# Kernel tuning notes

Hardware: AMD Instinct MI355X
Metric: run time of the kernel (lower is better)

## Reference

```python
import jax, jax.numpy as jnp
import numpy as np

N_NODES = 100000
N_EDGES = 1600000
DIM = 128
N_LAYERS = 4


def setup_inputs() -> dict:
    key = jax.random.key(0)
    ks = jax.random.split(key, 6)
    h = jax.random.normal(ks[0], (N_NODES, DIM), dtype=jnp.float32)
    src = jax.random.randint(ks[1], (N_EDGES,), 0, N_NODES, dtype=jnp.int32)
    dst = jax.random.randint(ks[2], (N_EDGES,), 0, N_NODES, dtype=jnp.int32)
    scale = 1.0 / np.sqrt(DIM)
    W_embed = jax.random.normal(ks[3], (DIM, DIM), dtype=jnp.float32) * scale
    b_embed = jnp.zeros((DIM,), dtype=jnp.float32)
    Ws = jax.random.normal(ks[4], (N_LAYERS, DIM, DIM), dtype=jnp.float32) * scale
    bs = jnp.zeros((N_LAYERS, DIM), dtype=jnp.float32)
    return {"h": h, "src": src, "dst": dst, "W_embed": W_embed,
            "b_embed": b_embed, "Ws": Ws, "bs": bs}


def reference(h, src, dst, W_embed, b_embed, Ws, bs):
    # Symmetric GCN normalization (DGL GraphConv norm='both'):
    # out-degree on src side, in-degree on dst side, clamped to >= 1.
    ones = jnp.ones(src.shape, h.dtype)
    deg_out = jax.ops.segment_sum(ones, src, num_segments=N_NODES)
    deg_in = jax.ops.segment_sum(ones, dst, num_segments=N_NODES)
    norm_s = jax.lax.rsqrt(jnp.maximum(deg_out, 1.0))  # [N]
    norm_d = jax.lax.rsqrt(jnp.maximum(deg_in, 1.0))   # [N]

    # embedding_h (dropout p=0 -> identity)
    h = h @ W_embed + b_embed

    for i in range(N_LAYERS):
        h_in = h
        # gather -> scale -> scatter-add (A_norm @ h)
        m = h[src] * norm_s[src, None]                              # [E, D]
        agg = jax.ops.segment_sum(m, dst, num_segments=N_NODES)    # [N, D]
        z = (agg * norm_d[:, None]) @ Ws[i] + bs[i]                 # GraphConv weight+bias
        z = jax.nn.relu(z)                                          # activation
        h = h_in + z                                                # residual
    return h
```

## Files before the change

kernel.cpp:

```cpp
#include <hip/hip_runtime.h>

#define DIMN 128
#define NLAYERS 4
#define KP 136
#define WTSH (2 * DIMN * KP)

#define BQL 9
#define BUCKW 512
#define BUCKCAP 10240
#define BSCH 4096
#define NBUK_MAX 256

#define HP_P 3
#define HP_C 48
#define HIST_BLOCKS (HP_P * HP_C)
#define HW_WORDS 16667

typedef __attribute__((ext_vector_type(8))) short bf16x8;
typedef __attribute__((ext_vector_type(4))) float f32x4;

__device__ inline float bfu2f(unsigned int u) { return __uint_as_float(u << 16); }
__device__ inline unsigned short f2bf(float f) {
    unsigned int u = __float_as_uint(f);
    return (unsigned short)((u + 0x7fffu + ((u >> 16) & 1u)) >> 16);
}
__device__ inline float blo(unsigned int u) { return __uint_as_float(u << 16); }
__device__ inline float bhi(unsigned int u) { return __uint_as_float(u & 0xffff0000u); }

__global__ __launch_bounds__(256) void k_pre(const int* __restrict__ src,
                                             const float* __restrict__ We,
                                             const float* __restrict__ Wlayers,
                                             unsigned int* __restrict__ degOutP,
                                             short* __restrict__ wt, int N, int E) {
    __shared__ unsigned int hsm[HW_WORDS];
    int tid = threadIdx.x;
    int bid = blockIdx.x;

    if (bid < HIST_BLOCKS) {
        int c = bid / HP_P;
        int p = bid % HP_P;
        int W = (N + 1) / 2;
        int w0 = p * HW_WORDS;
        int wn = min(HW_WORDS, W - w0);
        if (wn <= 0) return;
        int per = ((E + HP_C - 1) / HP_C + 3) & ~3;
        int e0 = c * per;
        int e1 = min(e0 + per, E);
        if (e0 >= e1) {
            for (int i = tid; i < wn; i += 256) degOutP[(size_t)c * W + w0 + i] = 0u;
            return;
        }
        for (int i = tid; i < wn; i += 256) hsm[i] = 0u;
        __syncthreads();
        int nvec = (e1 - e0) >> 2;
        const int4* sv = (const int4*)(src + e0);
        for (int it = tid; it < nvec; it += 256) {
            int4 v = sv[it];
            int w;
            w = (v.x >> 1) - w0; if ((unsigned)w < (unsigned)wn) atomicAdd(&hsm[w], 1u << ((v.x & 1) << 4));
            w = (v.y >> 1) - w0; if ((unsigned)w < (unsigned)wn) atomicAdd(&hsm[w], 1u << ((v.y & 1) << 4));
            w = (v.z >> 1) - w0; if ((unsigned)w < (unsigned)wn) atomicAdd(&hsm[w], 1u << ((v.z & 1) << 4));
            w = (v.w >> 1) - w0; if ((unsigned)w < (unsigned)wn) atomicAdd(&hsm[w], 1u << ((v.w & 1) << 4));
        }
        for (int j = e0 + (nvec << 2) + tid; j < e1; j += 256) {
            int s = src[j];
            int w = (s >> 1) - w0;
            if ((unsigned)w < (unsigned)wn) atomicAdd(&hsm[w], 1u << ((s & 1) << 4));
        }
        __syncthreads();
        for (int i = tid; i < wn; i += 256) degOutP[(size_t)c * W + w0 + i] = hsm[i];
        return;
    }

    {
        int m = bid - HIST_BLOCKS;
        const float* Wm = (m == 0) ? We : Wlayers + (size_t)(m - 1) * DIMN * DIMN;
        short* o = wt + (size_t)m * WTSH;
#pragma unroll
        for (int it = 0; it < 16; ++it) {
            int f = it * 1024 + tid * 4;
            float4 v = *(const float4*)(Wm + f);
            int k = f >> 7, n = f & 127;
            float vv[4] = {v.x, v.y, v.z, v.w};
#pragma unroll
            for (int j = 0; j < 4; ++j) {
                unsigned short hb = f2bf(vv[j]);
                float lo = vv[j] - bfu2f(hb);
                o[(n + j) * KP + k] = (short)hb;
                o[DIMN * KP + (n + j) * KP + k] = (short)f2bf(lo);
            }
        }
    }
}

__global__ __launch_bounds__(256) void k_binsort(const int* __restrict__ src,
                                                 const int* __restrict__ dst,
                                                 int* __restrict__ gcur,
                                                 int2* __restrict__ pairs,
                                                 int E, int NBUK) {
    __shared__ int cnt[NBUK_MAX];
    __shared__ int bofs[NBUK_MAX];
    __shared__ int gof[NBUK_MAX];
    __shared__ int scan_s[256];
    __shared__ int2 stg[BSCH];
    int tid = threadIdx.x;
    int e0 = blockIdx.x * BSCH;
    int n = min(BSCH, E - e0);
    if (n <= 0) return;
    cnt[tid] = 0;
    __syncthreads();

    int nv = n >> 2;
    const int4* dv4 = (const int4*)(dst + e0);
    for (int it = tid; it < nv; it += 256) {
        int4 d = dv4[it];
        atomicAdd(&cnt[d.x >> BQL], 1);
        atomicAdd(&cnt[d.y >> BQL], 1);
        atomicAdd(&cnt[d.z >> BQL], 1);
        atomicAdd(&cnt[d.w >> BQL], 1);
    }
    for (int j = (nv << 2) + tid; j < n; j += 256) {
        atomicAdd(&cnt[dst[e0 + j] >> BQL], 1);
    }
    __syncthreads();

    int myc = cnt[tid];
    scan_s[tid] = myc;
    __syncthreads();
    for (int off = 1; off < 256; off <<= 1) {
        int x = scan_s[tid];
        if (tid >= off) x += scan_s[tid - off];
        __syncthreads();
        scan_s[tid] = x;
        __syncthreads();
    }
    bofs[tid] = scan_s[tid] - myc;
    gof[tid] = (myc > 0 && tid < NBUK) ? atomicAdd(&gcur[tid], myc) : 0;
    cnt[tid] = 0;
    __syncthreads();

    const int4* sv4 = (const int4*)(src + e0);
    for (int it = tid; it < nv; it += 256) {
        int4 d = dv4[it];
        int4 s = sv4[it];
        int b, p;
        b = d.x >> BQL; p = bofs[b] + atomicAdd(&cnt[b], 1); stg[p] = make_int2(s.x, d.x);
        b = d.y >> BQL; p = bofs[b] + atomicAdd(&cnt[b], 1); stg[p] = make_int2(s.y, d.y);
        b = d.z >> BQL; p = bofs[b] + atomicAdd(&cnt[b], 1); stg[p] = make_int2(s.z, d.z);
        b = d.w >> BQL; p = bofs[b] + atomicAdd(&cnt[b], 1); stg[p] = make_int2(s.w, d.w);
    }
    for (int j = (nv << 2) + tid; j < n; j += 256) {
        int d = dst[e0 + j], s = src[e0 + j];
        int b = d >> BQL;
        int p = bofs[b] + atomicAdd(&cnt[b], 1);
        stg[p] = make_int2(s, d);
    }
    __syncthreads();

    for (int i = tid; i < n; i += 256) {
        int2 pr = stg[i];
        int b = pr.y >> BQL;
        int go = gof[b] + (i - bofs[b]);
        if (go < BUCKCAP) pairs[(size_t)b * BUCKCAP + go] = pr;
    }
}

__global__ __launch_bounds__(256) void k_build(const int2* __restrict__ pairs,
                                               const int* __restrict__ gcur,
                                               int* __restrict__ csr,
                                               int* __restrict__ rowptr,
                                               int* __restrict__ deg, int N) {
    int b = blockIdx.x;
    int tid = threadIdx.x;
    int cntb = gcur[b];
    if (cntb > BUCKCAP) cntb = BUCKCAP;
    __shared__ int c[BUCKW];
    __shared__ int pf[BUCKW];
    c[tid] = 0; c[tid + 256] = 0;
    __syncthreads();
    const int2* bp = pairs + (size_t)b * BUCKCAP;
    for (int i = tid; i < cntb; i += 256) atomicAdd(&c[bp[i].y & (BUCKW - 1)], 1);
    __syncthreads();
    pf[tid] = c[tid]; pf[tid + 256] = c[tid + 256];
    __syncthreads();
    for (int off = 1; off < BUCKW; off <<= 1) {
        int i0 = tid, i1 = tid + 256;
        int v0 = pf[i0] + ((i0 >= off) ? pf[i0 - off] : 0);
        int v1 = pf[i1] + ((i1 >= off) ? pf[i1 - off] : 0);
        __syncthreads();
        pf[i0] = v0; pf[i1] = v1;
        __syncthreads();
    }
    {
        int i0 = tid, i1 = tid + 256;
        int c0 = c[i0], c1 = c[i1];
        int ex0 = pf[i0] - c0, ex1 = pf[i1] - c1;
        pf[i0] = ex0; pf[i1] = ex1;
        int gn0 = (b << BQL) + i0, gn1 = (b << BQL) + i1;
        if (gn0 < N) { rowptr[gn0] = b * BUCKCAP + ex0; deg[gn0] = c0; }
        if (gn1 < N) { rowptr[gn1] = b * BUCKCAP + ex1; deg[gn1] = c1; }
        c[i0] = 0; c[i1] = 0;
    }
    __syncthreads();
    int* cb = csr + (size_t)b * BUCKCAP;
    for (int i = tid; i < cntb; i += 256) {
        int2 p = bp[i];
        int ld = p.y & (BUCKW - 1);
        int pos = pf[ld] + atomicAdd(&c[ld], 1);
        cb[pos] = p.x;
    }
}

__global__ __launch_bounds__(256) void k_norms(const int* __restrict__ deg,
                                               const unsigned int* __restrict__ degOutP,
                                               float* __restrict__ norm_d,
                                               float* __restrict__ norm_s, int N) {
    int i = blockIdx.x * 256 + threadIdx.x;
    int W = (N + 1) / 2;
    if (i < W) {
        unsigned s0 = 0, s1 = 0;
#pragma unroll 8
        for (int c = 0; c < HP_C; ++c) {
            unsigned v = degOutP[(size_t)c * W + i];
            s0 += v & 0xffffu;
            s1 += v >> 16;
        }
        int n0 = 2 * i, n1 = 2 * i + 1;
        norm_s[n0] = rsqrtf(fmaxf((float)s0, 1.0f));
        norm_d[n0] = rsqrtf(fmaxf((float)deg[n0], 1.0f));
        if (n1 < N) {
            norm_s[n1] = rsqrtf(fmaxf((float)s1, 1.0f));
            norm_d[n1] = rsqrtf(fmaxf((float)deg[n1], 1.0f));
        }
    }
}

__global__ __launch_bounds__(512) void k_gemm_f32(const float* __restrict__ A,
                                                  const short* __restrict__ Wt,
                                                  const float* __restrict__ bg,
                                                  float* __restrict__ tgt,
                                                  const float* __restrict__ norm_s,
                                                  unsigned short* __restrict__ Hs, int N) {
    __shared__ short Wl[WTSH];
    __shared__ float bias_s[DIMN];
    int tid = threadIdx.x;
    {
        const uint4* g = (const uint4*)Wt;
        uint4* l = (uint4*)Wl;
#pragma unroll
        for (int it = 0; it < 9; ++it) {
            int ix = it * 512 + tid;
            if (ix < WTSH / 8) l[ix] = g[ix];
        }
        if (tid < DIMN) bias_s[tid] = bg[tid];
    }
    __syncthreads();

    int lane = tid & 63;
    int wv = tid >> 6;
    int quad = lane >> 4;
    int l15 = lane & 15;
    int row0 = blockIdx.x * 256 + wv * 32;

    f32x4 acc[2][8];
#pragma unroll
    for (int s = 0; s < 2; ++s)
#pragma unroll
        for (int ct = 0; ct < 8; ++ct) acc[s][ct] = (f32x4){0.f, 0.f, 0.f, 0.f};

    for (int ks = 0; ks < 4; ++ks) {
        int kb = ks * 32 + quad * 8;
        bf16x8 ah[2], al[2];
#pragma unroll
        for (int s = 0; s < 2; ++s) {
            int r = row0 + s * 16 + l15;
            if (r > N - 1) r = N - 1;
            const float* ap = A + (size_t)r * DIMN + kb;
            float4 p = *(const float4*)ap;
            float4 q = *(const float4*)(ap + 4);
            float fv[8] = {p.x, p.y, p.z, p.w, q.x, q.y, q.z, q.w};
#pragma unroll
            for (int j = 0; j < 8; ++j) {
                unsigned short hb = f2bf(fv[j]);
                ah[s][j] = (short)hb;
                al[s][j] = (short)f2bf(fv[j] - bfu2f(hb));
            }
        }
#pragma unroll
        for (int ct = 0; ct < 8; ++ct) {
            const short* bp = Wl + (ct * 16 + l15) * KP + kb;
            bf16x8 bh = *(const bf16x8*)bp;
            bf16x8 bl = *(const bf16x8*)(bp + DIMN * KP);
#pragma unroll
            for (int s = 0; s < 2; ++s) {
                acc[s][ct] = __builtin_amdgcn_mfma_f32_16x16x32_bf16(ah[s], bh, acc[s][ct], 0, 0, 0);
                acc[s][ct] = __builtin_amdgcn_mfma_f32_16x16x32_bf16(al[s], bh, acc[s][ct], 0, 0, 0);
                acc[s][ct] = __builtin_amdgcn_mfma_f32_16x16x32_bf16(ah[s], bl, acc[s][ct], 0, 0, 0);
            }
        }
    }

#pragma unroll
    for (int s = 0; s < 2; ++s) {
        int rbase = row0 + s * 16 + quad * 4;
        float ns[4];
#pragma unroll
        for (int rj = 0; rj < 4; ++rj) {
            int row = rbase + rj;
            ns[rj] = (row < N) ? norm_s[row] : 0.f;
        }
#pragma unroll
        for (int ct = 0; ct < 8; ++ct) {
            int col = ct * 16 + l15;
            float bv = bias_s[col];
#pragma unroll
            for (int rj = 0; rj < 4; ++rj) {
                int row = rbase + rj;
                if (row < N) {
                    float o = acc[s][ct][rj] + bv;
                    __builtin_nontemporal_store(o, &tgt[(size_t)row * DIMN + col]);
                    Hs[(size_t)row * DIMN + col] = f2bf(o * ns[rj]);
                }
            }
        }
    }
}

__global__ __launch_bounds__(512) void k_gemm_bf(const unsigned short* __restrict__ A,
                                                 const short* __restrict__ Wt,
                                                 const float* __restrict__ bg,
                                                 const float* __restrict__ Hres,
                                                 float* __restrict__ tgt,
                                                 const float* __restrict__ norm_s,
                                                 unsigned short* __restrict__ Hs, int N) {
    __shared__ short Wl[WTSH];
    __shared__ float bias_s[DIMN];
    int tid = threadIdx.x;
    {
        const uint4* g = (const uint4*)Wt;
        uint4* l = (uint4*)Wl;
#pragma unroll
        for (int it = 0; it < 9; ++it) {
            int ix = it * 512 + tid;
            if (ix < WTSH / 8) l[ix] = g[ix];
        }
        if (tid < DIMN) bias_s[tid] = bg[tid];
    }
    __syncthreads();

    int lane = tid & 63;
    int wv = tid >> 6;
    int quad = lane >> 4;
    int l15 = lane & 15;
    int row0 = blockIdx.x * 256 + wv * 32;

    f32x4 acc[2][8];
#pragma unroll
    for (int s = 0; s < 2; ++s)
#pragma unroll
        for (int ct = 0; ct < 8; ++ct) acc[s][ct] = (f32x4){0.f, 0.f, 0.f, 0.f};

    for (int ks = 0; ks < 4; ++ks) {
        int kb = ks * 32 + quad * 8;
        bf16x8 ah[2];
#pragma unroll
        for (int s = 0; s < 2; ++s) {
            int r = row0 + s * 16 + l15;
            if (r > N - 1) r = N - 1;
            ah[s] = *(const bf16x8*)(A + (size_t)r * DIMN + kb);
        }
#pragma unroll
        for (int ct = 0; ct < 8; ++ct) {
            const short* bp = Wl + (ct * 16 + l15) * KP + kb;
            bf16x8 bh = *(const bf16x8*)bp;
            bf16x8 bl = *(const bf16x8*)(bp + DIMN * KP);
#pragma unroll
            for (int s = 0; s < 2; ++s) {
                acc[s][ct] = __builtin_amdgcn_mfma_f32_16x16x32_bf16(ah[s], bh, acc[s][ct], 0, 0, 0);
                acc[s][ct] = __builtin_amdgcn_mfma_f32_16x16x32_bf16(ah[s], bl, acc[s][ct], 0, 0, 0);
            }
        }
    }

    bool doHs = (Hs != nullptr);
#pragma unroll
    for (int s = 0; s < 2; ++s) {
        int rbase = row0 + s * 16 + quad * 4;
        float ns[4];
        if (doHs) {
#pragma unroll
            for (int rj = 0; rj < 4; ++rj) {
                int row = rbase + rj;
                ns[rj] = (row < N) ? norm_s[row] : 0.f;
            }
        }
#pragma unroll
        for (int ct = 0; ct < 8; ++ct) {
            int col = ct * 16 + l15;
            float bv = bias_s[col];
#pragma unroll
            for (int rj = 0; rj < 4; ++rj) {
                int row = rbase + rj;
                if (row < N) {
                    float o = fmaxf(acc[s][ct][rj] + bv, 0.f) + Hres[(size_t)row * DIMN + col];
                    __builtin_nontemporal_store(o, &tgt[(size_t)row * DIMN + col]);
                    if (doHs) Hs[(size_t)row * DIMN + col] = f2bf(o * ns[rj]);
                }
            }
        }
    }
}

__global__ __launch_bounds__(256) void k_spmm(const unsigned int* __restrict__ Hs,
                                              unsigned short* __restrict__ AggB,
                                              const int* __restrict__ csr,
                                              const int* __restrict__ rowptr,
                                              const int* __restrict__ deg,
                                              const float* __restrict__ norm_d, int N) {
    int wave = (blockIdx.x * blockDim.x + threadIdx.x) >> 6;
    int lane = threadIdx.x & 63;
    if (wave >= N) return;
    int cnt = deg[wave];
    const int* base = csr + rowptr[wave];
    int g = lane >> 5;
    int l5 = lane & 31;
    const uint2* H2 = (const uint2*)Hs;
    float4 acc = make_float4(0.f, 0.f, 0.f, 0.f);

    int emain = cnt & ~7;
    int e = 0;
    for (; e < emain; e += 8) {
        int s0 = base[e + g];
        int s1 = base[e + 2 + g];
        int s2 = base[e + 4 + g];
        int s3 = base[e + 6 + g];
        uint2 h0 = H2[(size_t)s0 * 32 + l5];
        uint2 h1 = H2[(size_t)s1 * 32 + l5];
        uint2 h2 = H2[(size_t)s2 * 32 + l5];
        uint2 h3 = H2[(size_t)s3 * 32 + l5];
        acc.x += blo(h0.x); acc.y += bhi(h0.x);
        acc.z += blo(h0.y); acc.w += bhi(h0.y);
        acc.x += blo(h1.x); acc.y += bhi(h1.x);
        acc.z += blo(h1.y); acc.w += bhi(h1.y);
        acc.x += blo(h2.x); acc.y += bhi(h2.x);
        acc.z += blo(h2.y); acc.w += bhi(h2.y);
        acc.x += blo(h3.x); acc.y += bhi(h3.x);
        acc.z += blo(h3.y); acc.w += bhi(h3.y);
    }
    for (; e < cnt; e += 2) {
        int ee = e + g;
        int sc = base[min(ee, cnt - 1)];
        uint2 hv = H2[(size_t)sc * 32 + l5];
        if (ee < cnt) {
            acc.x += blo(hv.x); acc.y += bhi(hv.x);
            acc.z += blo(hv.y); acc.w += bhi(hv.y);
        }
    }
    acc.x += __shfl_xor(acc.x, 32);
    acc.y += __shfl_xor(acc.y, 32);
    acc.z += __shfl_xor(acc.z, 32);
    acc.w += __shfl_xor(acc.w, 32);
    if (g == 0) {
        float nd = norm_d[wave];
        unsigned long long p =
            (unsigned long long)((unsigned)f2bf(acc.x * nd) | ((unsigned)f2bf(acc.y * nd) << 16)) |
            ((unsigned long long)((unsigned)f2bf(acc.z * nd) | ((unsigned)f2bf(acc.w * nd) << 16)) << 32);
        __builtin_nontemporal_store(p, &((unsigned long long*)AggB)[(size_t)wave * 32 + l5]);
    }
}

static inline char* align256(char* p) {
    return (char*)(((uintptr_t)p + 255) & ~(uintptr_t)255);
}

extern "C" void kernel_launch(void* const* d_in, const int* in_sizes, int n_in,
                              void* d_out, int out_size, void* d_ws, size_t ws_size,
                              hipStream_t stream) {
    const float* h_in = (const float*)d_in[0];
    const int* src = (const int*)d_in[1];
    const int* dst = (const int*)d_in[2];
    const float* W_embed = (const float*)d_in[3];
    const float* b_embed = (const float*)d_in[4];
    const float* Ws = (const float*)d_in[5];
    const float* bs = (const float*)d_in[6];
    float* out = (float*)d_out;

    const int N = in_sizes[0] / DIMN;
    const int E = in_sizes[1];
    const int W = (N + 1) / 2;
    const int NBUK = (N + BUCKW - 1) >> BQL;

    char* w = (char*)d_ws;
    float* Hc = (float*)w;               w = align256(w + (size_t)N * DIMN * 4);
    unsigned short* AggB = (unsigned short*)w; w = align256(w + (size_t)N * DIMN * 2);
    unsigned short* Hs = (unsigned short*)w;   w = align256(w + (size_t)N * DIMN * 2);
    int2* pairs = (int2*)w;              w = align256(w + (size_t)NBUK * BUCKCAP * 8);
    int* csr = (int*)w;                  w = align256(w + (size_t)NBUK * BUCKCAP * 4);
    int* rowptr = (int*)w;               w = align256(w + (size_t)N * 4);
    int* deg = (int*)w;                  w = align256(w + (size_t)N * 4);
    int* gcur = (int*)w;                 w = align256(w + (size_t)NBUK * 4);
    unsigned int* degOutP = (unsigned int*)w;  w = align256(w + (size_t)HP_C * W * 4);
    float* norm_s = (float*)w;           w = align256(w + (size_t)N * 4);
    float* norm_d = (float*)w;           w = align256(w + (size_t)N * 4);
    short* wt = (short*)w;               w = align256(w + (size_t)5 * WTSH * 2);

    (void)hipMemsetAsync(gcur, 0, (size_t)NBUK * 4, stream);

    int gb = (N + 255) / 256;
    int nb = (W + 255) / 256;
    int bb = (E + BSCH - 1) / BSCH;

    k_pre<<<HIST_BLOCKS + 5, 256, 0, stream>>>(src, W_embed, Ws, degOutP, wt, N, E);

    k_binsort<<<bb, 256, 0, stream>>>(src, dst, gcur, pairs, E, NBUK);
    k_build<<<NBUK, 256, 0, stream>>>(pairs, gcur, csr, rowptr, deg, N);

    k_norms<<<nb, 256, 0, stream>>>(deg, degOutP, norm_d, norm_s, N);

    k_gemm_f32<<<gb, 512, 0, stream>>>(h_in, wt, b_embed, Hc, norm_s, Hs, N);

    int sb = (N + 3) / 4;
    for (int l = 0; l < NLAYERS; ++l) {
        k_spmm<<<sb, 256, 0, stream>>>((const unsigned int*)Hs, AggB, csr, rowptr, deg, norm_d, N);
        float* tgt = (l == NLAYERS - 1) ? out : Hc;
        unsigned short* hs_next = (l == NLAYERS - 1) ? (unsigned short*)nullptr : Hs;
        k_gemm_bf<<<gb, 512, 0, stream>>>(AggB, wt + (size_t)(l + 1) * WTSH,
                                          bs + (size_t)l * DIMN, Hc, tgt, norm_s, hs_next, N);
    }
}
```

Measured before the change: 635.5 us.

## Fuse SpMM aggregation into per-layer GEMM kernel with ping-pong bf16 features

Each layer's gather-sum aggregation now runs inside the GEMM kernel. Every block of 128 rows aggregates its neighbours into a shared-memory tile and then runs the MFMA GEMM from LDS, which removes the separate spmm launch and the global round trip of the aggregated bf16 matrix. The low-part weights are stored in a new MFMA-friendly global layout and read from global or cache instead of LDS, which halves the LDS weight footprint so the aggregation tile fits. The bf16 feature buffers ping-pong to avoid read/write hazards. The cost is that the gather now runs at GEMM occupancy (512 threads with a large LDS use), and the GEMM waits on the slowest aggregation in each block.

```diff
diff --git a/kernel.cpp b/kernel.cpp
--- a/kernel.cpp
+++ b/kernel.cpp
@@ -4,6 +4,7 @@
 #define NLAYERS 4
 #define KP 136
 #define WTSH (2 * DIMN * KP)
+#define WTL_SH (DIMN * DIMN)
 
 #define BQL 9
 #define BUCKW 512
@@ -27,11 +28,16 @@
 __device__ inline float blo(unsigned int u) { return __uint_as_float(u << 16); }
 __device__ inline float bhi(unsigned int u) { return __uint_as_float(u & 0xffff0000u); }
 
+__device__ __host__ inline int lo_off(int n, int k) {
+    return ((((k >> 5) * 8 + (n >> 4)) * 16 + (n & 15)) * 4 + ((k >> 3) & 3)) * 8 + (k & 7);
+}
+
 __global__ __launch_bounds__(256) void k_pre(const int* __restrict__ src,
                                              const float* __restrict__ We,
                                              const float* __restrict__ Wlayers,
                                              unsigned int* __restrict__ degOutP,
-                                             short* __restrict__ wt, int N, int E) {
+                                             short* __restrict__ wt,
+                                             short* __restrict__ wtl, int N, int E) {
     __shared__ unsigned int hsm[HW_WORDS];
     int tid = threadIdx.x;
     int bid = blockIdx.x;
@@ -76,6 +82,7 @@
         int m = bid - HIST_BLOCKS;
         const float* Wm = (m == 0) ? We : Wlayers + (size_t)(m - 1) * DIMN * DIMN;
         short* o = wt + (size_t)m * WTSH;
+        short* ol = wtl + (size_t)m * WTL_SH;
 #pragma unroll
         for (int it = 0; it < 16; ++it) {
             int f = it * 1024 + tid * 4;
@@ -86,8 +93,10 @@
             for (int j = 0; j < 4; ++j) {
                 unsigned short hb = f2bf(vv[j]);
                 float lo = vv[j] - bfu2f(hb);
+                unsigned short lb = f2bf(lo);
                 o[(n + j) * KP + k] = (short)hb;
-                o[DIMN * KP + (n + j) * KP + k] = (short)f2bf(lo);
+                o[DIMN * KP + (n + j) * KP + k] = (short)lb;
+                ol[lo_off(n + j, k)] = (short)lb;
             }
         }
     }
@@ -326,23 +335,30 @@
     }
 }
 
-__global__ __launch_bounds__(512) void k_gemm_bf(const unsigned short* __restrict__ A,
-                                                 const short* __restrict__ Wt,
-                                                 const float* __restrict__ bg,
-                                                 const float* __restrict__ Hres,
-                                                 float* __restrict__ tgt,
-                                                 const float* __restrict__ norm_s,
-                                                 unsigned short* __restrict__ Hs, int N) {
-    __shared__ short Wl[WTSH];
+__global__ __launch_bounds__(512) void k_layer(const unsigned int* __restrict__ HsIn,
+                                               const int* __restrict__ csr,
+                                               const int* __restrict__ rowptr,
+                                               const int* __restrict__ deg,
+                                               const float* __restrict__ norm_d,
+                                               const short* __restrict__ Wt,
+                                               const short* __restrict__ Wtl,
+                                               const float* __restrict__ bg,
+                                               const float* __restrict__ Hres,
+                                               float* __restrict__ tgt,
+                                               const float* __restrict__ norm_s,
+                                               unsigned short* __restrict__ HsOut,
+                                               int N) {
+    __shared__ short Wl[DIMN * KP];
+    __shared__ short Ag[128 * KP];
     __shared__ float bias_s[DIMN];
     int tid = threadIdx.x;
     {
-        const uint4* g = (const uint4*)Wt;
-        uint4* l = (uint4*)Wl;
-#pragma unroll
-        for (int it = 0; it < 9; ++it) {
+        const uint4* g4 = (const uint4*)Wt;
+        uint4* l4 = (uint4*)Wl;
+#pragma unroll
+        for (int it = 0; it < 5; ++it) {
             int ix = it * 512 + tid;
-            if (ix < WTSH / 8) l[ix] = g[ix];
+            if (ix < (DIMN * KP) / 8) l4[ix] = g4[ix];
         }
         if (tid < DIMN) bias_s[tid] = bg[tid];
     }
@@ -352,120 +368,102 @@
     int wv = tid >> 6;
     int quad = lane >> 4;
     int l15 = lane & 15;
-    int row0 = blockIdx.x * 256 + wv * 32;
-
-    f32x4 acc[2][8];
-#pragma unroll
-    for (int s = 0; s < 2; ++s)
-#pragma unroll
-        for (int ct = 0; ct < 8; ++ct) acc[s][ct] = (f32x4){0.f, 0.f, 0.f, 0.f};
+    int row0 = blockIdx.x * 128;
+
+    {
+        int g = lane >> 5;
+        int l5 = lane & 31;
+        const uint2* H2 = (const uint2*)HsIn;
+        for (int i = 0; i < 16; ++i) {
+            int node = row0 + wv * 16 + i;
+            float4 acc = make_float4(0.f, 0.f, 0.f, 0.f);
+            if (node < N) {
+                int cnt = deg[node];
+                const int* base = csr + rowptr[node];
+                int emain = cnt & ~7;
+                int e = 0;
+                for (; e < emain; e += 8) {
+                    int s0 = base[e + g];
+                    int s1 = base[e + 2 + g];
+                    int s2 = base[e + 4 + g];
+                    int s3 = base[e + 6 + g];
+                    uint2 h0 = H2[(size_t)s0 * 32 + l5];
+                    uint2 h1 = H2[(size_t)s1 * 32 + l5];
+                    uint2 h2 = H2[(size_t)s2 * 32 + l5];
+                    uint2 h3 = H2[(size_t)s3 * 32 + l5];
+                    acc.x += blo(h0.x); acc.y += bhi(h0.x);
+                    acc.z += blo(h0.y); acc.w += bhi(h0.y);
+                    acc.x += blo(h1.x); acc.y += bhi(h1.x);
+                    acc.z += blo(h1.y); acc.w += bhi(h1.y);
+                    acc.x += blo(h2.x); acc.y += bhi(h2.x);
+                    acc.z += blo(h2.y); acc.w += bhi(h2.y);
+                    acc.x += blo(h3.x); acc.y += bhi(h3.x);
+                    acc.z += blo(h3.y); acc.w += bhi(h3.y);
+                }
+                for (; e < cnt; e += 2) {
+                    int ee = e + g;
+                    int sc = base[min(ee, cnt - 1)];
+                    uint2 hv = H2[(size_t)sc * 32 + l5];
+                    if (ee < cnt) {
+                        acc.x += blo(hv.x); acc.y += bhi(hv.x);
+                        acc.z += blo(hv.y); acc.w += bhi(hv.y);
+                    }
+                }
+            }
+            acc.x += __shfl_xor(acc.x, 32);
+            acc.y += __shfl_xor(acc.y, 32);
+            acc.z += __shfl_xor(acc.z, 32);
+            acc.w += __shfl_xor(acc.w, 32);
+            if (g == 0) {
+                float nd = (node < N) ? norm_d[node] : 0.f;
+                unsigned long long p =
+                    (unsigned long long)((unsigned)f2bf(acc.x * nd) | ((unsigned)f2bf(acc.y * nd) << 16)) |
+                    ((unsigned long long)((unsigned)f2bf(acc.z * nd) | ((unsigned)f2bf(acc.w * nd) << 16)) << 32);
+                *(unsigned long long*)&Ag[(size_t)(wv * 16 + i) * KP + l5 * 4] = p;
+            }
+        }
+    }
+
+    f32x4 acc[8];
+#pragma unroll
+    for (int ct = 0; ct < 8; ++ct) acc[ct] = (f32x4){0.f, 0.f, 0.f, 0.f};
 
     for (int ks = 0; ks < 4; ++ks) {
         int kb = ks * 32 + quad * 8;
-        bf16x8 ah[2];
-#pragma unroll
-        for (int s = 0; s < 2; ++s) {
-            int r = row0 + s * 16 + l15;
-            if (r > N - 1) r = N - 1;
-            ah[s] = *(const bf16x8*)(A + (size_t)r * DIMN + kb);
-        }
+        bf16x8 ah = *(const bf16x8*)&Ag[(wv * 16 + l15) * KP + kb];
 #pragma unroll
         for (int ct = 0; ct < 8; ++ct) {
             const short* bp = Wl + (ct * 16 + l15) * KP + kb;
             bf16x8 bh = *(const bf16x8*)bp;
-            bf16x8 bl = *(const bf16x8*)(bp + DIMN * KP);
-#pragma unroll
-            for (int s = 0; s < 2; ++s) {
-                acc[s][ct] = __builtin_amdgcn_mfma_f32_16x16x32_bf16(ah[s], bh, acc[s][ct], 0, 0, 0);
-                acc[s][ct] = __builtin_amdgcn_mfma_f32_16x16x32_bf16(ah[s], bl, acc[s][ct], 0, 0, 0);
-            }
-        }
-    }
-
-    bool doHs = (Hs != nullptr);
-#pragma unroll
-    for (int s = 0; s < 2; ++s) {
-        int rbase = row0 + s * 16 + quad * 4;
-        float ns[4];
-        if (doHs) {
-#pragma unroll
-            for (int rj = 0; rj < 4; ++rj) {
-                int row = rbase + rj;
-                ns[rj] = (row < N) ? norm_s[row] : 0.f;
-            }
-        }
-#pragma unroll
-        for (int ct = 0; ct < 8; ++ct) {
-            int col = ct * 16 + l15;
-            float bv = bias_s[col];
-#pragma unroll
-            for (int rj = 0; rj < 4; ++rj) {
-                int row = rbase + rj;
-                if (row < N) {
-                    float o = fmaxf(acc[s][ct][rj] + bv, 0.f) + Hres[(size_t)row * DIMN + col];
-                    __builtin_nontemporal_store(o, &tgt[(size_t)row * DIMN + col]);
-                    if (doHs) Hs[(size_t)row * DIMN + col] = f2bf(o * ns[rj]);
-                }
-            }
-        }
-    }
-}
-
-__global__ __launch_bounds__(256) void k_spmm(const unsigned int* __restrict__ Hs,
-                                              unsigned short* __restrict__ AggB,
-                                              const int* __restrict__ csr,
-                                              const int* __restrict__ rowptr,
-                                              const int* __restrict__ deg,
-                                              const float* __restrict__ norm_d, int N) {
-    int wave = (blockIdx.x * blockDim.x + threadIdx.x) >> 6;
-    int lane = threadIdx.x & 63;
-    if (wave >= N) return;
-    int cnt = deg[wave];
-    const int* base = csr + rowptr[wave];
-    int g = lane >> 5;
-    int l5 = lane & 31;
-    const uint2* H2 = (const uint2*)Hs;
-    float4 acc = make_float4(0.f, 0.f, 0.f, 0.f);
-
-    int emain = cnt & ~7;
-    int e = 0;
-    for (; e < emain; e += 8) {
-        int s0 = base[e + g];
-        int s1 = base[e + 2 + g];
-        int s2 = base[e + 4 + g];
-        int s3 = base[e + 6 + g];
-        uint2 h0 = H2[(size_t)s0 * 32 + l5];
-        uint2 h1 = H2[(size_t)s1 * 32 + l5];
-        uint2 h2 = H2[(size_t)s2 * 32 + l5];
-        uint2 h3 = H2[(size_t)s3 * 32 + l5];
-        acc.x += blo(h0.x); acc.y += bhi(h0.x);
-        acc.z += blo(h0.y); acc.w += bhi(h0.y);
-        acc.x += blo(h1.x); acc.y += bhi(h1.x);
-        acc.z += blo(h1.y); acc.w += bhi(h1.y);
-        acc.x += blo(h2.x); acc.y += bhi(h2.x);
-        acc.z += blo(h2.y); acc.w += bhi(h2.y);
-        acc.x += blo(h3.x); acc.y += bhi(h3.x);
-        acc.z += blo(h3.y); acc.w += bhi(h3.y);
-    }
-    for (; e < cnt; e += 2) {
-        int ee = e + g;
-        int sc = base[min(ee, cnt - 1)];
-        uint2 hv = H2[(size_t)sc * 32 + l5];
-        if (ee < cnt) {
-            acc.x += blo(hv.x); acc.y += bhi(hv.x);
-            acc.z += blo(hv.y); acc.w += bhi(hv.y);
-        }
-    }
-    acc.x += __shfl_xor(acc.x, 32);
-    acc.y += __shfl_xor(acc.y, 32);
-    acc.z += __shfl_xor(acc.z, 32);
-    acc.w += __shfl_xor(acc.w, 32);
-    if (g == 0) {
-        float nd = norm_d[wave];
-        unsigned long long p =
-            (unsigned long long)((unsigned)f2bf(acc.x * nd) | ((unsigned)f2bf(acc.y * nd) << 16)) |
-            ((unsigned long long)((unsigned)f2bf(acc.z * nd) | ((unsigned)f2bf(acc.w * nd) << 16)) << 32);
-        __builtin_nontemporal_store(p, &((unsigned long long*)AggB)[(size_t)wave * 32 + l5]);
+            bf16x8 bl = *(const bf16x8*)(Wtl + ((ks * 8 + ct) * 16 + l15) * 32 + quad * 8);
+            acc[ct] = __builtin_amdgcn_mfma_f32_16x16x32_bf16(ah, bh, acc[ct], 0, 0, 0);
+            acc[ct] = __builtin_amdgcn_mfma_f32_16x16x32_bf16(ah, bl, acc[ct], 0, 0, 0);
+        }
+    }
+
+    bool doHs = (HsOut != nullptr);
+    int rbase = row0 + wv * 16 + quad * 4;
+    float ns[4];
+    if (doHs) {
+#pragma unroll
+        for (int rj = 0; rj < 4; ++rj) {
+            int row = rbase + rj;
+            ns[rj] = (row < N) ? norm_s[row] : 0.f;
+        }
+    }
+#pragma unroll
+    for (int ct = 0; ct < 8; ++ct) {
+        int col = ct * 16 + l15;
+        float bv = bias_s[col];
+#pragma unroll
+        for (int rj = 0; rj < 4; ++rj) {
+            int row = rbase + rj;
+            if (row < N) {
+                float o = fmaxf(acc[ct][rj] + bv, 0.f) + Hres[(size_t)row * DIMN + col];
+                __builtin_nontemporal_store(o, &tgt[(size_t)row * DIMN + col]);
+                if (doHs) HsOut[(size_t)row * DIMN + col] = f2bf(o * ns[rj]);
+            }
+        }
     }
 }
 
@@ -492,8 +490,8 @@
 
     char* w = (char*)d_ws;
     float* Hc = (float*)w;               w = align256(w + (size_t)N * DIMN * 4);
-    unsigned short* AggB = (unsigned short*)w; w = align256(w + (size_t)N * DIMN * 2);
-    unsigned short* Hs = (unsigned short*)w;   w = align256(w + (size_t)N * DIMN * 2);
+    unsigned short* HsA = (unsigned short*)w;  w = align256(w + (size_t)N * DIMN * 2);
+    unsigned short* HsB = (unsigned short*)w;  w = align256(w + (size_t)N * DIMN * 2);
     int2* pairs = (int2*)w;              w = align256(w + (size_t)NBUK * BUCKCAP * 8);
     int* csr = (int*)w;                  w = align256(w + (size_t)NBUK * BUCKCAP * 4);
     int* rowptr = (int*)w;               w = align256(w + (size_t)N * 4);
@@ -503,28 +501,33 @@
     float* norm_s = (float*)w;           w = align256(w + (size_t)N * 4);
     float* norm_d = (float*)w;           w = align256(w + (size_t)N * 4);
     short* wt = (short*)w;               w = align256(w + (size_t)5 * WTSH * 2);
+    short* wtl = (short*)w;              w = align256(w + (size_t)5 * WTL_SH * 2);
 
     (void)hipMemsetAsync(gcur, 0, (size_t)NBUK * 4, stream);
 
-    int gb = (N + 255) / 256;
+    int gb256 = (N + 255) / 256;
+    int gb128 = (N + 127) / 128;
     int nb = (W + 255) / 256;
     int bb = (E + BSCH - 1) / BSCH;
 
-    k_pre<<<HIST_BLOCKS + 5, 256, 0, stream>>>(src, W_embed, Ws, degOutP, wt, N, E);
+    k_pre<<<HIST_BLOCKS + 5, 256, 0, stream>>>(src, W_embed, Ws, degOutP, wt, wtl, N, E);
 
     k_binsort<<<bb, 256, 0, stream>>>(src, dst, gcur, pairs, E, NBUK);
     k_build<<<NBUK, 256, 0, stream>>>(pairs, gcur, csr, rowptr, deg, N);
 
     k_norms<<<nb, 256, 0, stream>>>(deg, degOutP, norm_d, norm_s, N);
 
-    k_gemm_f32<<<gb, 512, 0, stream>>>(h_in, wt, b_embed, Hc, norm_s, Hs, N);
-
-    int sb = (N + 3) / 4;
+    k_gemm_f32<<<gb256, 512, 0, stream>>>(h_in, wt, b_embed, Hc, norm_s, HsA, N);
+
+    unsigned short* hs_in = HsA;
+    unsigned short* hs_out = HsB;
     for (int l = 0; l < NLAYERS; ++l) {
-        k_spmm<<<sb, 256, 0, stream>>>((const unsigned int*)Hs, AggB, csr, rowptr, deg, norm_d, N);
         float* tgt = (l == NLAYERS - 1) ? out : Hc;
-        unsigned short* hs_next = (l == NLAYERS - 1) ? (unsigned short*)nullptr : Hs;
-        k_gemm_bf<<<gb, 512, 0, stream>>>(AggB, wt + (size_t)(l + 1) * WTSH,
-                                          bs + (size_t)l * DIMN, Hc, tgt, norm_s, hs_next, N);
-    }
-}
+        unsigned short* ho = (l == NLAYERS - 1) ? (unsigned short*)nullptr : hs_out;
+        k_layer<<<gb128, 512, 0, stream>>>((const unsigned int*)hs_in, csr, rowptr, deg,
+                                           norm_d, wt + (size_t)(l + 1) * WTSH,
+                                           wtl + (size_t)(l + 1) * WTL_SH,
+                                           bs + (size_t)l * DIMN, Hc, tgt, norm_s, ho, N);
+        unsigned short* t = hs_in; hs_in = hs_out; hs_out = t;
+    }
+}
```

New measurement: 835.3 us. +31.4%, slower.
